# Kernel tuning notes

Hardware: AMD Instinct MI355X
Metric: run time of the kernel (lower is better)

Reference implementation:

```python
import jax, jax.numpy as jnp
import numpy as np

N_DIM = 768
HIDDEN_DIM = 768
BATCH = 4
SEQ = 2048


def setup_inputs() -> dict:
    key = jax.random.key(0)
    ks = jax.random.split(key, 9)
    s_in = 1.0 / np.sqrt(N_DIM)
    s_h = 1.0 / np.sqrt(HIDDEN_DIM)
    return {
        "x": jax.random.normal(ks[0], (BATCH, SEQ, N_DIM), dtype=jnp.float32),
        # torch Linear weights: [out_features, in_features]
        "wq": jax.random.uniform(ks[1], (HIDDEN_DIM, N_DIM), jnp.float32, -s_in, s_in),
        "bq": jax.random.uniform(ks[2], (HIDDEN_DIM,), jnp.float32, -s_in, s_in),
        "wk": jax.random.uniform(ks[3], (HIDDEN_DIM, N_DIM), jnp.float32, -s_in, s_in),
        "bk": jax.random.uniform(ks[4], (HIDDEN_DIM,), jnp.float32, -s_in, s_in),
        "wv": jax.random.uniform(ks[5], (HIDDEN_DIM, N_DIM), jnp.float32, -s_in, s_in),
        "bv": jax.random.uniform(ks[6], (HIDDEN_DIM,), jnp.float32, -s_in, s_in),
        "wo": jax.random.uniform(ks[7], (N_DIM, HIDDEN_DIM), jnp.float32, -s_h, s_h),
        "bo": jax.random.uniform(ks[8], (N_DIM,), jnp.float32, -s_h, s_h),
    }


def reference(x, wq, bq, wk, bk, wv, bv, wo, bo):
    # q,k,v: [B, S, H]
    q = jnp.einsum("bsd,hd->bsh", x, wq) + bq
    k = jnp.einsum("bsd,hd->bsh", x, wk) + bk
    v = jnp.einsum("bsd,hd->bsh", x, wv) + bv
    # NOTE: faithful to source — no 1/sqrt(d) scaling, no mask.
    scores = jnp.einsum("bqh,bkh->bqk", q, k)  # [B, S, S]
    attn = jax.nn.softmax(scores, axis=-1)
    y = jnp.einsum("bqk,bkh->bqh", attn, v)  # [B, S, H]
    out = jnp.einsum("bsh,dh->bsd", y, wo) + bo
    return out
```

## Files before the change

### kernel.cpp

```cpp
#include <hip/hip_runtime.h>

typedef _Float16 f16;
typedef _Float16 f16x8 __attribute__((ext_vector_type(8)));
typedef float f32x4 __attribute__((ext_vector_type(4)));

#define GLD16(g, l) __builtin_amdgcn_global_load_lds( \
    (const __attribute__((address_space(1))) void*)(g), \
    (__attribute__((address_space(3))) void*)(l), 16, 0, 0)

template <typename OutT, int BM, int BN, int MODE, int MINW>
__global__ __launch_bounds__(256, MINW)
void gemm_kernel(const f16* __restrict__ A, long sA,
                 const f16* __restrict__ B, long sB,
                 void* __restrict__ Cv, long sC,
                 void* __restrict__ C2v,
                 const float* __restrict__ bias,
                 const float* __restrict__ bias2,
                 int N, int K,
                 const f16* __restrict__ A2,
                 const f16* __restrict__ B2,
                 void* __restrict__ C3v)
{
    constexpr int FM = BM / 32;
    constexpr int FN = BN / 32;
    constexpr int IA = BM / 32;
    constexpr int IB = BN / 32;

    OutT* C  = (OutT*)Cv;
    OutT* C2 = (OutT*)C2v;
    const int tid  = threadIdx.x;
    const int wave = tid >> 6;
    const int lane = tid & 63;
    const int bz   = blockIdx.z;

    const f16* Ab = A + (long)bz * sA;
    const f16* Bb = B + (long)bz * sB;
    C += (long)bz * sC;
    int Kk = K;
    long bm, bn;
    bool sub = false;
    if (MODE == 3 && blockIdx.y == gridDim.y - 1) {
        if (blockIdx.x >= 36) return;
        sub = true;
        Ab = A2; Bb = B2; Kk = 768;
        bm = (long)(blockIdx.x / 6) * BM;
        bn = (long)(blockIdx.x % 6) * BN;
    } else {
        bm = (long)blockIdx.x * BM;
        bn = (long)blockIdx.y * BN;
    }

    __shared__ f16 sAt[BM * 64];
    __shared__ f16 sBt[BN * 64];

    const int srow = lane >> 3;
    const int gch  = ((lane & 7) ^ srow) * 8;

    const f16* gAb = Ab + (bm + wave * (BM / 4) + srow) * (long)Kk + gch;
    const f16* gBb = Bb + (bn + wave * (BN / 4) + srow) * (long)Kk + gch;

    const int wm = (wave >> 1) * (BM / 2);
    const int wn = (wave & 1) * (BN / 2);
    const int lr = lane & 15;
    const int qd = lane >> 4;
    const int swz0 = ((0 * 4 + qd) ^ (lr & 7)) * 8;
    const int swz1 = ((1 * 4 + qd) ^ (lr & 7)) * 8;

    f32x4 acc[FM][FN] = {};

    for (int k0 = 0; k0 < Kk; k0 += 64) {
        #pragma unroll
        for (int i = 0; i < IA; ++i)
            GLD16(gAb + k0 + (long)i * 8 * Kk, &sAt[(wave * (BM / 4) + i * 8) * 64]);
        #pragma unroll
        for (int i = 0; i < IB; ++i)
            GLD16(gBb + k0 + (long)i * 8 * Kk, &sBt[(wave * (BN / 4) + i * 8) * 64]);
        __syncthreads();

        #pragma unroll
        for (int h = 0; h < 2; ++h) {
            const int swz = h ? swz1 : swz0;
            f16x8 af[FM], bf[FN];
            #pragma unroll
            for (int t = 0; t < FM; ++t)
                af[t] = *(const f16x8*)&sAt[(wm + t * 16 + lr) * 64 + swz];
            #pragma unroll
            for (int t = 0; t < FN; ++t)
                bf[t] = *(const f16x8*)&sBt[(wn + t * 16 + lr) * 64 + swz];
            #pragma unroll
            for (int tm = 0; tm < FM; ++tm)
                #pragma unroll
                for (int tn = 0; tn < FN; ++tn)
                    acc[tm][tn] = __builtin_amdgcn_mfma_f32_16x16x32_f16(
                        af[tm], bf[tn], acc[tm][tn], 0, 0, 0);
        }
        __syncthreads();
    }

    if (MODE == 3 && sub) {
        f16* W = (f16*)C3v;
        #pragma unroll
        for (int tn = 0; tn < FN; ++tn) {
            const long col = bn + wn + tn * 16 + lr;
            #pragma unroll
            for (int tm = 0; tm < FM; ++tm)
                #pragma unroll
                for (int r = 0; r < 4; ++r) {
                    const long row = bm + wm + tm * 16 + qd * 4 + r;
                    W[row * 768 + col] = (f16)acc[tm][tn][r];
                }
        }
        return;
    }
    #pragma unroll
    for (int tn = 0; tn < FN; ++tn) {
        const long col = bn + wn + tn * 16 + lr;
        OutT* dst = C;
        long cc = col, stride = N;
        float bc = 0.f;
        if (MODE == 1) bc = bias[col];
        if (MODE == 3) {
            stride = 768;
            if (col >= 768) { dst = C2; cc = col - 768; bc = bias2[cc]; }
            else            { bc = bias[cc]; }
        }
        #pragma unroll
        for (int tm = 0; tm < FM; ++tm) {
            #pragma unroll
            for (int r = 0; r < 4; ++r) {
                const long row = bm + wm + tm * 16 + qd * 4 + r;
                float v = acc[tm][tn][r] + bc;
                if (MODE == 2) v += bias[row];
                dst[row * stride + cc] = (OutT)v;
            }
        }
    }
}

__global__ __launch_bounds__(256)
void softmax_kernel(f16* __restrict__ S)
{
    const long row = blockIdx.x;
    f16* p = S + row * 2048;
    const int tid  = threadIdx.x;
    const int wave = tid >> 6;
    const int lane = tid & 63;

    f16x8 x = *(const f16x8*)&p[tid * 8];
    float v[8];
    float m = -1e30f;
    #pragma unroll
    for (int j = 0; j < 8; ++j) { v[j] = (float)x[j]; m = fmaxf(m, v[j]); }
    #pragma unroll
    for (int off = 32; off > 0; off >>= 1) m = fmaxf(m, __shfl_down(m, off));

    __shared__ float rm[4], rs[4];
    if (lane == 0) rm[wave] = m;
    __syncthreads();
    m = fmaxf(fmaxf(rm[0], rm[1]), fmaxf(rm[2], rm[3]));

    float s = 0.f;
    #pragma unroll
    for (int j = 0; j < 8; ++j) { v[j] = __expf(v[j] - m); s += v[j]; }
    #pragma unroll
    for (int off = 32; off > 0; off >>= 1) s += __shfl_down(s, off);
    if (lane == 0) rs[wave] = s;
    __syncthreads();
    s = rs[0] + rs[1] + rs[2] + rs[3];
    const float inv = 1.0f / s;

    f16x8 y;
    #pragma unroll
    for (int j = 0; j < 8; ++j) y[j] = (f16)(v[j] * inv);
    *(f16x8*)&p[tid * 8] = y;
}

__global__ __launch_bounds__(256)
void cvt_all_kernel(const float* __restrict__ x,
                    const float* __restrict__ wq, const float* __restrict__ wk,
                    const float* __restrict__ wv, const float* __restrict__ wo,
                    const float* __restrict__ bv,
                    f16* __restrict__ x16, f16* __restrict__ w16,
                    f16* __restrict__ wvT, float* __restrict__ cB)
{
    __shared__ f16 t[64][72];
    const int b = blockIdx.x;
    const int tid = threadIdx.x;

    if (b < 3936) {
        const float* in; f16* out; long i;
        if (b < 3072) {
            in = x; out = x16;
            i = ((long)b * 256 + tid) * 8;
        } else {
            const int wb  = b - 3072;
            const int sel = wb / 288;
            in  = (sel == 0) ? wq : (sel == 1) ? wk : wo;
            out = w16 + (long)((sel == 2) ? 3 : sel) * 589824;
            i = ((long)(wb - sel * 288) * 256 + tid) * 8;
        }
        float4 a = *(const float4*)(in + i);
        float4 c = *(const float4*)(in + i + 4);
        f16x8 o;
        o[0] = (f16)a.x; o[1] = (f16)a.y; o[2] = (f16)a.z; o[3] = (f16)a.w;
        o[4] = (f16)c.x; o[5] = (f16)c.y; o[6] = (f16)c.z; o[7] = (f16)c.w;
        *(f16x8*)&out[i] = o;
    } else if (b < 4080) {
        const int tb = b - 3936;
        const int tr = tb / 12, tc = tb % 12;
        const int r  = tid >> 2;
        const int c0 = (tid & 3) * 16;
        const float* src = wv + ((long)tr * 64 + r) * 768 + tc * 64 + c0;
        float4 a0 = *(const float4*)(src);
        float4 a1 = *(const float4*)(src + 4);
        float4 a2 = *(const float4*)(src + 8);
        float4 a3 = *(const float4*)(src + 12);
        f16 vv[16];
        vv[0]=(f16)a0.x; vv[1]=(f16)a0.y; vv[2]=(f16)a0.z; vv[3]=(f16)a0.w;
        vv[4]=(f16)a1.x; vv[5]=(f16)a1.y; vv[6]=(f16)a1.z; vv[7]=(f16)a1.w;
        vv[8]=(f16)a2.x; vv[9]=(f16)a2.y; vv[10]=(f16)a2.z; vv[11]=(f16)a2.w;
        vv[12]=(f16)a3.x; vv[13]=(f16)a3.y; vv[14]=(f16)a3.z; vv[15]=(f16)a3.w;
        f16* wv16 = w16 + (long)2 * 589824;
        f16x8 o1, o2;
        #pragma unroll
        for (int i = 0; i < 8; ++i) { o1[i] = vv[i]; o2[i] = vv[8 + i]; }
        f16* d16 = wv16 + ((long)tr * 64 + r) * 768 + tc * 64 + c0;
        *(f16x8*)d16 = o1;
        *(f16x8*)(d16 + 8) = o2;
        #pragma unroll
        for (int i = 0; i < 16; ++i) t[r][c0 + i] = vv[i];
        __syncthreads();
        #pragma unroll
        for (int i = 0; i < 8; ++i) { o1[i] = t[c0 + i][r]; o2[i] = t[c0 + 8 + i][r]; }
        f16* dT = wvT + ((long)tc * 64 + r) * 768 + tr * 64 + c0;
        *(f16x8*)dT = o1;
        *(f16x8*)(dT + 8) = o2;
    } else {
        const int d0 = (b - 4080) * 64;
        const int wave = tid >> 6, lane = tid & 63;
        for (int it = 0; it < 16; ++it) {
            const int d = d0 + it * 4 + wave;
            float s = 0.f;
            #pragma unroll
            for (int j = 0; j < 12; ++j) {
                const int h = lane + 64 * j;
                s += wo[(long)d * 768 + h] * bv[h];
            }
            #pragma unroll
            for (int off = 32; off > 0; off >>= 1) s += __shfl_down(s, off);
            if (lane == 0) cB[d] = s;
        }
    }
}

extern "C" void kernel_launch(void* const* d_in, const int* in_sizes, int n_in,
                              void* d_out, int out_size, void* d_ws, size_t ws_size,
                              hipStream_t stream)
{
    const float* x  = (const float*)d_in[0];
    const float* wq = (const float*)d_in[1];
    const float* bq = (const float*)d_in[2];
    const float* wk = (const float*)d_in[3];
    const float* bk = (const float*)d_in[4];
    const float* wv = (const float*)d_in[5];
    const float* bv = (const float*)d_in[6];
    const float* wo = (const float*)d_in[7];
    const float* bo = (const float*)d_in[8];

    char* ws = (char*)d_ws;
    f16* x16  = (f16*)(ws + 0);
    f16* w16  = (f16*)(ws + 12582912);
    f16* Q    = (f16*)(ws + 17301504);
    f16* Kb   = (f16*)(ws + 29884416);
    f16* VWT  = (f16*)(ws + 42467328);
    f16* S    = (f16*)(ws + 55050240);
    f16* wvT  = (f16*)(ws + 88604672);
    f16* Wc   = (f16*)(ws + 89784320);
    float* cB = (float*)(ws + 90963968);

    f16* wo16 = w16 + 3 * 589824;

    cvt_all_kernel<<<4092, 256, 0, stream>>>(x, wq, wk, wv, wo, bv,
                                             x16, w16, wvT, cB);
    gemm_kernel<f16, 128, 128, 3, 3><<<dim3(64, 13, 1), 256, 0, stream>>>(
        x16, 0, w16, 0, Q, 0, Kb, bq, bk, 1536, 768, wo16, wvT, Wc);
    gemm_kernel<f16, 64, 128, 2, 4><<<dim3(12, 16, 4), 256, 0, stream>>>(
        Wc, 0, x16, (long)2048 * 768, VWT, (long)768 * 2048, nullptr,
        cB, nullptr, 2048, 768, nullptr, nullptr, nullptr);
    gemm_kernel<f16, 128, 256, 0, 2><<<dim3(16, 8, 4), 256, 0, stream>>>(
        Q, (long)2048 * 768, Kb, (long)2048 * 768, S, (long)2048 * 2048,
        nullptr, nullptr, nullptr, 2048, 768, nullptr, nullptr, nullptr);
    softmax_kernel<<<8192, 256, 0, stream>>>(S);
    gemm_kernel<float, 128, 64, 1, 4><<<dim3(16, 12, 4), 256, 0, stream>>>(
        S, (long)2048 * 2048, VWT, (long)768 * 2048, d_out, (long)2048 * 768,
        nullptr, bo, nullptr, 768, 2048, nullptr, nullptr, nullptr);
}
```

Before: 228.0 us.

## Merge VW GEMM into QK^T scores launch and flatten grids to 1D jobs

The separate launch that computes VWT (Wc times x, plus the combined bias) now runs as extra tail blocks of the QK^T scores GEMM. One 1D grid of 704 blocks covers both jobs, each using a 128x256 tile. The QKV-projection launch is also flattened to a 1D grid of 804 blocks so the Wo·Wv sub-job no longer wastes empty blocks. This removes one kernel launch and its tail, letting the two independent GEMMs fill the GPU together. The trade-off is that the VW job now uses the larger tile with lower occupancy, which may balance worse.

```diff
diff --git a/kernel.cpp b/kernel.cpp
--- a/kernel.cpp
+++ b/kernel.cpp
@@ -19,35 +19,62 @@
                  int N, int K,
                  const f16* __restrict__ A2,
                  const f16* __restrict__ B2,
-                 void* __restrict__ C3v)
+                 void* __restrict__ C3v,
+                 const float* __restrict__ bias3)
 {
     constexpr int FM = BM / 32;
     constexpr int FN = BN / 32;
     constexpr int IA = BM / 32;
     constexpr int IB = BN / 32;
 
-    OutT* C  = (OutT*)Cv;
-    OutT* C2 = (OutT*)C2v;
     const int tid  = threadIdx.x;
     const int wave = tid >> 6;
     const int lane = tid & 63;
-    const int bz   = blockIdx.z;
-
-    const f16* Ab = A + (long)bz * sA;
-    const f16* Bb = B + (long)bz * sB;
-    C += (long)bz * sC;
-    int Kk = K;
+
+    const f16* Ab;
+    const f16* Bb;
     long bm, bn;
-    bool sub = false;
-    if (MODE == 3 && blockIdx.y == gridDim.y - 1) {
-        if (blockIdx.x >= 36) return;
-        sub = true;
-        Ab = A2; Bb = B2; Kk = 768;
-        bm = (long)(blockIdx.x / 6) * BM;
-        bn = (long)(blockIdx.x % 6) * BN;
+    long czoff = 0;
+    int  job = 0;
+
+    if (MODE == 4) {
+        const int idx = blockIdx.x;
+        if (idx < 768) {
+            Ab = A; Bb = B;
+            bm = (long)(idx & 63) * BM;
+            bn = (long)(idx >> 6) * BN;
+        } else {
+            job = 1;
+            const int t = idx - 768;
+            Ab = A2; Bb = B2;
+            bm = (long)(t / 6) * BM;
+            bn = (long)(t % 6) * BN;
+        }
+    } else if (MODE == 5) {
+        const int idx = blockIdx.x;
+        if (idx < 512) {
+            const int sz = idx >> 7, r = idx & 127;
+            Ab = A + (long)sz * 1572864;
+            Bb = B + (long)sz * 1572864;
+            bm = (long)(r & 15) * BM;
+            bn = (long)(r >> 4) * BN;
+            czoff = (long)sz * 4194304;
+        } else {
+            job = 1;
+            const int t = idx - 512;
+            const int vz = t / 48, r = t % 48;
+            Ab = A2;
+            Bb = B2 + (long)vz * 1572864;
+            bm = (long)(r % 6) * BM;
+            bn = (long)(r / 6) * BN;
+            czoff = (long)vz * 1572864;
+        }
     } else {
+        Ab = A + (long)blockIdx.z * sA;
+        Bb = B + (long)blockIdx.z * sB;
         bm = (long)blockIdx.x * BM;
         bn = (long)blockIdx.y * BN;
+        czoff = (long)blockIdx.z * sC;
     }
 
     __shared__ f16 sAt[BM * 64];
@@ -56,8 +83,8 @@
     const int srow = lane >> 3;
     const int gch  = ((lane & 7) ^ srow) * 8;
 
-    const f16* gAb = Ab + (bm + wave * (BM / 4) + srow) * (long)Kk + gch;
-    const f16* gBb = Bb + (bn + wave * (BN / 4) + srow) * (long)Kk + gch;
+    const f16* gAb = Ab + (bm + wave * (BM / 4) + srow) * (long)K + gch;
+    const f16* gBb = Bb + (bn + wave * (BN / 4) + srow) * (long)K + gch;
 
     const int wm = (wave >> 1) * (BM / 2);
     const int wn = (wave & 1) * (BN / 2);
@@ -68,13 +95,13 @@
 
     f32x4 acc[FM][FN] = {};
 
-    for (int k0 = 0; k0 < Kk; k0 += 64) {
+    for (int k0 = 0; k0 < K; k0 += 64) {
         #pragma unroll
         for (int i = 0; i < IA; ++i)
-            GLD16(gAb + k0 + (long)i * 8 * Kk, &sAt[(wave * (BM / 4) + i * 8) * 64]);
+            GLD16(gAb + k0 + (long)i * 8 * K, &sAt[(wave * (BM / 4) + i * 8) * 64]);
         #pragma unroll
         for (int i = 0; i < IB; ++i)
-            GLD16(gBb + k0 + (long)i * 8 * Kk, &sBt[(wave * (BN / 4) + i * 8) * 64]);
+            GLD16(gBb + k0 + (long)i * 8 * K, &sBt[(wave * (BN / 4) + i * 8) * 64]);
         __syncthreads();
 
         #pragma unroll
@@ -97,41 +124,83 @@
         __syncthreads();
     }
 
-    if (MODE == 3 && sub) {
-        f16* W = (f16*)C3v;
+    if (MODE == 4) {
+        if (job == 1) {
+            f16* W = (f16*)C3v;
+            #pragma unroll
+            for (int tn = 0; tn < FN; ++tn) {
+                const long col = bn + wn + tn * 16 + lr;
+                #pragma unroll
+                for (int tm = 0; tm < FM; ++tm)
+                    #pragma unroll
+                    for (int r = 0; r < 4; ++r) {
+                        const long row = bm + wm + tm * 16 + qd * 4 + r;
+                        W[row * 768 + col] = (f16)acc[tm][tn][r];
+                    }
+            }
+            return;
+        }
+        f16* Qd = (f16*)Cv;
+        f16* Kd = (f16*)C2v;
         #pragma unroll
         for (int tn = 0; tn < FN; ++tn) {
             const long col = bn + wn + tn * 16 + lr;
+            f16* dst = Qd;
+            long cc = col;
+            float bc;
+            if (col >= 768) { dst = Kd; cc = col - 768; bc = bias2[cc]; }
+            else            { bc = bias[cc]; }
             #pragma unroll
             for (int tm = 0; tm < FM; ++tm)
                 #pragma unroll
                 for (int r = 0; r < 4; ++r) {
                     const long row = bm + wm + tm * 16 + qd * 4 + r;
-                    W[row * 768 + col] = (f16)acc[tm][tn][r];
+                    dst[row * 768 + cc] = (f16)(acc[tm][tn][r] + bc);
                 }
         }
         return;
     }
+    if (MODE == 5) {
+        if (job == 1) {
+            f16* W = (f16*)C3v + czoff;
+            #pragma unroll
+            for (int tn = 0; tn < FN; ++tn) {
+                const long col = bn + wn + tn * 16 + lr;
+                #pragma unroll
+                for (int tm = 0; tm < FM; ++tm)
+                    #pragma unroll
+                    for (int r = 0; r < 4; ++r) {
+                        const long row = bm + wm + tm * 16 + qd * 4 + r;
+                        W[row * 2048 + col] = (f16)(acc[tm][tn][r] + bias3[row]);
+                    }
+            }
+            return;
+        }
+        f16* W = (f16*)Cv + czoff;
+        #pragma unroll
+        for (int tn = 0; tn < FN; ++tn) {
+            const long col = bn + wn + tn * 16 + lr;
+            #pragma unroll
+            for (int tm = 0; tm < FM; ++tm)
+                #pragma unroll
+                for (int r = 0; r < 4; ++r) {
+                    const long row = bm + wm + tm * 16 + qd * 4 + r;
+                    W[row * 2048 + col] = (f16)acc[tm][tn][r];
+                }
+        }
+        return;
+    }
+    OutT* C = (OutT*)Cv + czoff;
     #pragma unroll
     for (int tn = 0; tn < FN; ++tn) {
         const long col = bn + wn + tn * 16 + lr;
-        OutT* dst = C;
-        long cc = col, stride = N;
-        float bc = 0.f;
-        if (MODE == 1) bc = bias[col];
-        if (MODE == 3) {
-            stride = 768;
-            if (col >= 768) { dst = C2; cc = col - 768; bc = bias2[cc]; }
-            else            { bc = bias[cc]; }
-        }
+        float bc = (MODE == 1) ? bias[col] : 0.f;
         #pragma unroll
         for (int tm = 0; tm < FM; ++tm) {
             #pragma unroll
             for (int r = 0; r < 4; ++r) {
                 const long row = bm + wm + tm * 16 + qd * 4 + r;
-                float v = acc[tm][tn][r] + bc;
-                if (MODE == 2) v += bias[row];
-                dst[row * stride + cc] = (OutT)v;
+                C[row * (long)N + col] = (OutT)(acc[tm][tn][r] + bc);
             }
         }
     }
@@ -282,16 +351,13 @@
 
     cvt_all_kernel<<<4092, 256, 0, stream>>>(x, wq, wk, wv, wo, bv,
                                              x16, w16, wvT, cB);
-    gemm_kernel<f16, 128, 128, 3, 3><<<dim3(64, 13, 1), 256, 0, stream>>>(
-        x16, 0, w16, 0, Q, 0, Kb, bq, bk, 1536, 768, wo16, wvT, Wc);
-    gemm_kernel<f16, 64, 128, 2, 4><<<dim3(12, 16, 4), 256, 0, stream>>>(
-        Wc, 0, x16, (long)2048 * 768, VWT, (long)768 * 2048, nullptr,
-        cB, nullptr, 2048, 768, nullptr, nullptr, nullptr);
-    gemm_kernel<f16, 128, 256, 0, 2><<<dim3(16, 8, 4), 256, 0, stream>>>(
-        Q, (long)2048 * 768, Kb, (long)2048 * 768, S, (long)2048 * 2048,
-        nullptr, nullptr, nullptr, 2048, 768, nullptr, nullptr, nullptr);
+    gemm_kernel<f16, 128, 128, 4, 3><<<804, 256, 0, stream>>>(
+        x16, 0, w16, 0, Q, 0, Kb, bq, bk, 1536, 768, wo16, wvT, Wc, nullptr);
+    gemm_kernel<f16, 128, 256, 5, 2><<<704, 256, 0, stream>>>(
+        Q, 0, Kb, 0, S, 0, nullptr, nullptr, nullptr, 2048, 768,
+        Wc, x16, VWT, cB);
     softmax_kernel<<<8192, 256, 0, stream>>>(S);
     gemm_kernel<float, 128, 64, 1, 4><<<dim3(16, 12, 4), 256, 0, stream>>>(
         S, (long)2048 * 2048, VWT, (long)768 * 2048, d_out, (long)2048 * 768,
-        nullptr, bo, nullptr, 768, 2048, nullptr, nullptr, nullptr);
+        nullptr, bo, nullptr, 768, 2048, nullptr, nullptr, nullptr, nullptr);
 }
```

Result: no change. 227.8 us (-0.1%).
